# Kernel tuning notes

Measured on AMD Instinct MI355X. Metric: run time of the kernel, lower is better.

The kernel has to match this reference:

```python
import jax, jax.numpy as jnp
import numpy as np

NUM_LAYERS = 2
NUM_RES_LAYERS = 1  # residual add applied to layers i >= NUM_LAYERS - NUM_RES_LAYERS


def _lstm_seq(x, W, U, b, reverse):
    """Keras-style LSTM over full sequence. x:[B,T,E], W:[E,4H], U:[H,4H], b:[4H].
    Gate order i,f,g,o (Keras). reverse=True emulates go_backwards + K.reverse
    (lax.scan reverse=True keeps outputs time-aligned). Returns [B,T,H]."""
    B = x.shape[0]
    H = U.shape[0]
    # precompute input projections for all timesteps in one big matmul
    zx = jnp.einsum('bte,eg->btg', x, W) + b  # [B,T,4H]
    zx = jnp.swapaxes(zx, 0, 1)  # [T,B,4H]

    def step(carry, zxt):
        h, c = carry
        z = zxt + h @ U  # [B,4H]
        i, f, g, o = jnp.split(z, 4, axis=-1)
        i = jax.nn.sigmoid(i)
        f = jax.nn.sigmoid(f)
        g = jnp.tanh(g)
        o = jax.nn.sigmoid(o)
        c = f * c + i * g
        h = o * jnp.tanh(c)
        return (h, c), h

    init = (jnp.zeros((B, H), x.dtype), jnp.zeros((B, H), x.dtype))
    _, hs = jax.lax.scan(step, init, zx, reverse=reverse)  # [T,B,H]
    return jnp.swapaxes(hs, 0, 1)


def setup_inputs() -> dict:
    key = jax.random.key(0)
    k1, k2, k3 = jax.random.split(key, 3)
    B, T, E, H = 512, 200, 128, 128
    s = 0.05  # keep gates in a sane regime
    x = jax.random.normal(k1, (B, T, E), dtype=jnp.float32)
    W = jax.random.normal(k2, (NUM_LAYERS, 2, E, 4 * H), dtype=jnp.float32) * s
    U = jax.random.normal(k3, (NUM_LAYERS, 2, H, 4 * H), dtype=jnp.float32) * s
    b = jnp.ones((NUM_LAYERS, 2, 4 * H), dtype=jnp.float32)  # bias_initializer='ones'
    return {"x": x, "W": W, "U": U, "b": b}


def reference(x, W, U, b):
    # inference mode: dropout inactive
    input_fw = x
    input_bw = x
    for i in range(NUM_LAYERS):
        out_fw = _lstm_seq(input_fw, W[i, 0], U[i, 0], b[i, 0], reverse=False)
        out_bw = _lstm_seq(input_bw, W[i, 1], U[i, 1], b[i, 1], reverse=True)
        if i >= NUM_LAYERS - NUM_RES_LAYERS:
            out_fw = out_fw + input_fw
            out_bw = out_bw + input_bw
        input_fw = out_fw
        input_bw = out_bw
    # mode == 'ave'
    return (input_fw + input_bw) / 2
```

## Files before the change

kernel.cpp:

```cpp
#include <hip/hip_runtime.h>


typedef _Float16 f16;
typedef _Float16 f16x4 __attribute__((ext_vector_type(4)));
typedef _Float16 f16x8 __attribute__((ext_vector_type(8)));
typedef float    f32x4 __attribute__((ext_vector_type(4)));

#define B_   512
#define T_   200
#define E_   128
#define H_   128
#define G4_  512
#define M_   (B_*T_)

static __device__ __forceinline__ float rcpf_(float x) {
#if __has_builtin(__builtin_amdgcn_rcpf)
  return __builtin_amdgcn_rcpf(x);
#else
  return 1.f / x;
#endif
}
static __device__ __forceinline__ float sigm(float x) { return rcpf_(1.f + __expf(-x)); }
static __device__ __forceinline__ float tanh_(float x) { return 2.f * rcpf_(1.f + __expf(-2.f * x)) - 1.f; }

static __device__ __forceinline__ void lgkm_barrier() {
  asm volatile("s_waitcnt lgkmcnt(0)" ::: "memory");
  __builtin_amdgcn_s_barrier();
}

__global__ __launch_bounds__(256)
void cvt_x(const float* __restrict__ x, f16* __restrict__ xh) {
  const int n8 = M_ * E_ / 8;
  for (int i = blockIdx.x * 256 + threadIdx.x; i < n8; i += gridDim.x * 256) {
    const float4 a = ((const float4*)x)[i * 2];
    const float4 b = ((const float4*)x)[i * 2 + 1];
    f16x8 v;
    v[0] = (f16)a.x; v[1] = (f16)a.y; v[2] = (f16)a.z; v[3] = (f16)a.w;
    v[4] = (f16)b.x; v[5] = (f16)b.y; v[6] = (f16)b.z; v[7] = (f16)b.w;
    *(f16x8*)(xh + (size_t)i * 8) = v;
  }
}

__global__ __launch_bounds__(256)
void prep_w(const float* __restrict__ W, const float* __restrict__ U,
            f16* __restrict__ Wt, f16* __restrict__ Ut) {
  const int m = blockIdx.x;
  const float* s = (m < 4 ? W + (size_t)m * E_ * G4_ : U + (size_t)(m - 4) * E_ * G4_);
  f16* d        = (m < 4 ? Wt + (size_t)m * E_ * G4_ : Ut + (size_t)(m - 4) * E_ * G4_);
  for (int i = threadIdx.x; i < E_ * G4_; i += 256) {
    const int k = i >> 9, g = i & 511;
    d[(size_t)g * E_ + k] = (f16)s[i];
  }
}

template <int LAYER>
__global__ __launch_bounds__(512, 2)
void scan_fused(const f16* __restrict__ in,
                const f16* __restrict__ Utl,
                const f16* __restrict__ Wtl,
                const float* __restrict__ bl,
                const f16* __restrict__ res,
                f16* __restrict__ hout)
{
  __shared__ f16 hsh[2][16][136];

  const int tid  = threadIdx.x;
  const int lane = tid & 63;
  const int wv   = tid >> 6;
  const int row  = lane & 15;
  const int kg   = lane >> 4;
  const int bx   = blockIdx.x;
  const int dir  = bx >> 5;
  const int R0   = (bx & 31) * 16;
  const int coff = wv * 16 + kg * 4;

  const f16* Ud = Utl + (size_t)dir * G4_ * E_;
  const f16* Wd = Wtl + (size_t)dir * G4_ * E_;
  const float* bd = bl + (size_t)dir * G4_;
  const f16* ind  = in + (LAYER == 1 ? (size_t)dir * M_ * H_ : 0);
  f16* houtd      = hout + (size_t)dir * M_ * H_;

  f16x8 aU[4][4], aW[4][4];
#pragma unroll
  for (int g = 0; g < 4; ++g) {
    const size_t gcol = (size_t)(g * 128 + wv * 16 + row) * E_;
#pragma unroll
    for (int kk = 0; kk < 4; ++kk) {
      aU[g][kk] = *(const f16x8*)(Ud + gcol + kk * 32 + kg * 8);
      aW[g][kk] = *(const f16x8*)(Wd + gcol + kk * 32 + kg * 8);
    }
  }
  f32x4 zb[4];
#pragma unroll
  for (int g = 0; g < 4; ++g) {
#pragma unroll
    for (int i = 0; i < 4; ++i) zb[g][i] = bd[g * 128 + coff + i];
  }

  for (int i = tid; i < 2 * 16 * 136; i += 512) ((f16*)hsh)[i] = (f16)0.f;

  const int t0 = dir ? (T_ - 1) : 0;
  const int ts = dir ? -1 : 1;

  const f16* inrow  = ind + (size_t)(R0 + row) * T_ * E_;
  const f16* resrow = (LAYER == 1)
      ? res + (size_t)dir * M_ * H_ + (size_t)(R0 + row) * T_ * H_ : nullptr;
  f16* outrow = houtd + (size_t)(R0 + row) * T_ * H_;

  float cc[4] = {0.f, 0.f, 0.f, 0.f};

  f16x8 xA[4], xB[4];
  f16x4 rvA = {}, rvB = {};
  {
    const f16* pA = inrow + (size_t)t0 * E_;
    const f16* pB = inrow + (size_t)(t0 + ts) * E_;
#pragma unroll
    for (int kk = 0; kk < 4; ++kk) {
      xA[kk] = *(const f16x8*)(pA + kk * 32 + kg * 8);
      xB[kk] = *(const f16x8*)(pB + kk * 32 + kg * 8);
    }
    if (LAYER == 1) {
      rvA = *(const f16x4*)(resrow + (size_t)t0 * H_ + coff);
      rvB = *(const f16x4*)(resrow + (size_t)(t0 + ts) * H_ + coff);
    }
  }

  lgkm_barrier();

  auto step = [&](f16x8 (&xp)[4], f16x4& rv, int s, int rp, int wp) {
    const int t = t0 + s * ts;

    f16x8 hf[4];
#pragma unroll
    for (int kk = 0; kk < 4; ++kk) hf[kk] = *(const f16x8*)&hsh[rp][row][kk * 32 + kg * 8];

    f16x8 xf[4];
#pragma unroll
    for (int kk = 0; kk < 4; ++kk) xf[kk] = xp[kk];
    float rvf[4];
    if (LAYER == 1) {
#pragma unroll
      for (int i = 0; i < 4; ++i) rvf[i] = (float)rv[i];
    }

    {
      const int spf = s + 2;
      const size_t tpf = (spf < T_) ? (size_t)(t0 + spf * ts) : (size_t)t0;
      const f16* p = inrow + tpf * E_;
#pragma unroll
      for (int kk = 0; kk < 4; ++kk) xp[kk] = *(const f16x8*)(p + kk * 32 + kg * 8);
      if (LAYER == 1) rv = *(const f16x4*)(resrow + tpf * H_ + coff);
    }

    f32x4 z0 = zb[0], z1 = zb[1], z2 = zb[2], z3 = zb[3];
#pragma unroll
    for (int kk = 0; kk < 4; ++kk) {
      z0 = __builtin_amdgcn_mfma_f32_16x16x32_f16(aW[0][kk], xf[kk], z0, 0, 0, 0);
      z1 = __builtin_amdgcn_mfma_f32_16x16x32_f16(aW[1][kk], xf[kk], z1, 0, 0, 0);
      z2 = __builtin_amdgcn_mfma_f32_16x16x32_f16(aW[2][kk], xf[kk], z2, 0, 0, 0);
      z3 = __builtin_amdgcn_mfma_f32_16x16x32_f16(aW[3][kk], xf[kk], z3, 0, 0, 0);
    }
#pragma unroll
    for (int kk = 0; kk < 4; ++kk) {
      z0 = __builtin_amdgcn_mfma_f32_16x16x32_f16(aU[0][kk], hf[kk], z0, 0, 0, 0);
      z1 = __builtin_amdgcn_mfma_f32_16x16x32_f16(aU[1][kk], hf[kk], z1, 0, 0, 0);
      z2 = __builtin_amdgcn_mfma_f32_16x16x32_f16(aU[2][kk], hf[kk], z2, 0, 0, 0);
      z3 = __builtin_amdgcn_mfma_f32_16x16x32_f16(aU[3][kk], hf[kk], z3, 0, 0, 0);
    }

    float hv[4];
#pragma unroll
    for (int i = 0; i < 4; ++i) {
      const float ig = sigm(z0[i]);
      const float fg = sigm(z1[i]);
      const float gg = tanh_(z2[i]);
      const float og = sigm(z3[i]);
      cc[i] = fg * cc[i] + ig * gg;
      hv[i] = og * tanh_(cc[i]);
    }
    f16x4 hp;
#pragma unroll
    for (int i = 0; i < 4; ++i) hp[i] = (f16)hv[i];
    *(f16x4*)&hsh[wp][row][coff] = hp;

    f16* orow = outrow + (size_t)t * H_ + coff;
    if (LAYER == 0) {
      *(f16x4*)orow = hp;
    } else {
      f16x4 o;
#pragma unroll
      for (int i = 0; i < 4; ++i) o[i] = (f16)(0.5f * (hv[i] + rvf[i]));
      *(f16x4*)orow = o;
    }

    lgkm_barrier();
  };

  for (int k = 0; k < T_ / 2; ++k) {
    step(xA, rvA, 2 * k,     0, 1);
    step(xB, rvB, 2 * k + 1, 1, 0);
  }
}

__global__ __launch_bounds__(256)
void final_add(const f16* __restrict__ a, const f16* __restrict__ b,
               float* __restrict__ o)
{
  const int n8 = M_ * H_ / 8;
  for (int i = blockIdx.x * 256 + threadIdx.x; i < n8; i += gridDim.x * 256) {
    const f16x8 va = *(const f16x8*)(a + (size_t)i * 8);
    const f16x8 vb = *(const f16x8*)(b + (size_t)i * 8);
    float4 o0, o1;
    o0.x = (float)va[0] + (float)vb[0];  o0.y = (float)va[1] + (float)vb[1];
    o0.z = (float)va[2] + (float)vb[2];  o0.w = (float)va[3] + (float)vb[3];
    o1.x = (float)va[4] + (float)vb[4];  o1.y = (float)va[5] + (float)vb[5];
    o1.z = (float)va[6] + (float)vb[6];  o1.w = (float)va[7] + (float)vb[7];
    *(float4*)(o + (size_t)i * 8)     = o0;
    *(float4*)(o + (size_t)i * 8 + 4) = o1;
  }
}

extern "C" void kernel_launch(void* const* d_in, const int* in_sizes, int n_in,
                              void* d_out, int out_size, void* d_ws, size_t ws_size,
                              hipStream_t stream) {
  const float* x = (const float*)d_in[0];
  const float* W = (const float*)d_in[1];
  const float* U = (const float*)d_in[2];
  const float* b = (const float*)d_in[3];
  float* out = (float*)d_out;

  char* ws = (char*)d_ws;
  f16* xh = (f16*)ws;
  f16* h0 = xh + (size_t)M_ * E_;
  f16* h1 = h0 + (size_t)2 * M_ * H_;
  f16* Wt = h1 + (size_t)2 * M_ * H_;
  f16* Ut = Wt + (size_t)4 * G4_ * E_;

  const size_t WTL = (size_t)2 * G4_ * E_;
  const size_t BL  = 2 * G4_;

  cvt_x<<<dim3(2048), 256, 0, stream>>>(x, xh);
  prep_w<<<dim3(8), 256, 0, stream>>>(W, U, Wt, Ut);
  scan_fused<0><<<dim3(64), 512, 0, stream>>>(xh, Ut, Wt, b, nullptr, h0);
  scan_fused<1><<<dim3(64), 512, 0, stream>>>(h0, Ut + WTL, Wt + WTL, b + BL, h0, h1);
  final_add<<<dim3(2048), 256, 0, stream>>>(h1, h1 + (size_t)M_ * H_, out);
}
```

Before: 684.8 us.

## Replace gate transcendentals with shared-memory sigmoid LUT and pipeline input projection

Gate activations now come from an 8192-entry sigmoid lookup table in LDS, built per block, instead of exp and reciprocal. tanh is expressed as 2*sigmoid(2x)-1, with the g-gate weights and bias pre-scaled by 2. The input-projection MFMAs for the next step are issued right after the current step's recurrent MFMAs, so they sit off the serial dependency chain. The nearest-entry lookup with a 1/256 step adds approximation error and possible LDS bank conflicts, and the prefetch can read past the sequence edge, which the workspace offset seems meant to absorb.

```diff
diff --git a/kernel.cpp b/kernel.cpp
--- a/kernel.cpp
+++ b/kernel.cpp
@@ -1,4 +1,5 @@
 #include <hip/hip_runtime.h>
+#include <math.h>
 
 
 typedef _Float16 f16;
@@ -12,16 +13,7 @@
 #define H_   128
 #define G4_  512
 #define M_   (B_*T_)
-
-static __device__ __forceinline__ float rcpf_(float x) {
-#if __has_builtin(__builtin_amdgcn_rcpf)
-  return __builtin_amdgcn_rcpf(x);
-#else
-  return 1.f / x;
-#endif
-}
-static __device__ __forceinline__ float sigm(float x) { return rcpf_(1.f + __expf(-x)); }
-static __device__ __forceinline__ float tanh_(float x) { return 2.f * rcpf_(1.f + __expf(-2.f * x)) - 1.f; }
+#define LUTN 8192
 
 static __device__ __forceinline__ void lgkm_barrier() {
   asm volatile("s_waitcnt lgkmcnt(0)" ::: "memory");
@@ -49,7 +41,9 @@
   f16* d        = (m < 4 ? Wt + (size_t)m * E_ * G4_ : Ut + (size_t)(m - 4) * E_ * G4_);
   for (int i = threadIdx.x; i < E_ * G4_; i += 256) {
     const int k = i >> 9, g = i & 511;
-    d[(size_t)g * E_ + k] = (f16)s[i];
+    float v = s[i];
+    if ((g >> 7) == 2) v *= 2.f;
+    d[(size_t)g * E_ + k] = (f16)v;
   }
 }
 
@@ -62,6 +56,7 @@
                 const f16* __restrict__ res,
                 f16* __restrict__ hout)
 {
+  __shared__ float lut[LUTN];
   __shared__ f16 hsh[2][16][136];
 
   const int tid  = threadIdx.x;
@@ -80,6 +75,12 @@
   const f16* ind  = in + (LAYER == 1 ? (size_t)dir * M_ * H_ : 0);
   f16* houtd      = hout + (size_t)dir * M_ * H_;
 
+  for (int i = tid; i < LUTN; i += 512) {
+    const float xx = (float)(i - LUTN / 2) * (1.f / 256.f);
+    lut[i] = 1.f / (1.f + expf(-xx));
+  }
+  for (int i = tid; i < 2 * 16 * 136; i += 512) ((f16*)hsh)[i] = (f16)0.f;
+
   f16x8 aU[4][4], aW[4][4];
 #pragma unroll
   for (int g = 0; g < 4; ++g) {
@@ -94,10 +95,11 @@
 #pragma unroll
   for (int g = 0; g < 4; ++g) {
 #pragma unroll
-    for (int i = 0; i < 4; ++i) zb[g][i] = bd[g * 128 + coff + i];
-  }
-
-  for (int i = tid; i < 2 * 16 * 136; i += 512) ((f16*)hsh)[i] = (f16)0.f;
+    for (int i = 0; i < 4; ++i) {
+      const float v = bd[g * 128 + coff + i];
+      zb[g][i] = (g == 2) ? 2.f * v : v;
+    }
+  }
 
   const int t0 = dir ? (T_ - 1) : 0;
   const int ts = dir ? -1 : 1;
@@ -109,81 +111,92 @@
 
   float cc[4] = {0.f, 0.f, 0.f, 0.f};
 
-  f16x8 xA[4], xB[4];
+  f16x8 xP[4], xA[4], xB[4];
   f16x4 rvA = {}, rvB = {};
-  {
-    const f16* pA = inrow + (size_t)t0 * E_;
-    const f16* pB = inrow + (size_t)(t0 + ts) * E_;
+#pragma unroll
+  for (int kk = 0; kk < 4; ++kk) {
+    xP[kk] = *(const f16x8*)(inrow + (long)t0 * E_ + kk * 32 + kg * 8);
+    xA[kk] = *(const f16x8*)(inrow + (long)(t0 + ts) * E_ + kk * 32 + kg * 8);
+    xB[kk] = *(const f16x8*)(inrow + (long)(t0 + 2 * ts) * E_ + kk * 32 + kg * 8);
+  }
+  if (LAYER == 1) {
+    rvA = *(const f16x4*)(resrow + (long)t0 * H_ + coff);
+    rvB = *(const f16x4*)(resrow + (long)(t0 + ts) * H_ + coff);
+  }
+
+  lgkm_barrier();
+
+  f32x4 zA[4], zB[4];
+#pragma unroll
+  for (int g = 0; g < 4; ++g) zA[g] = zb[g];
+#pragma unroll
+  for (int kk = 0; kk < 4; ++kk) {
+    zA[0] = __builtin_amdgcn_mfma_f32_16x16x32_f16(aW[0][kk], xP[kk], zA[0], 0, 0, 0);
+    zA[1] = __builtin_amdgcn_mfma_f32_16x16x32_f16(aW[1][kk], xP[kk], zA[1], 0, 0, 0);
+    zA[2] = __builtin_amdgcn_mfma_f32_16x16x32_f16(aW[2][kk], xP[kk], zA[2], 0, 0, 0);
+    zA[3] = __builtin_amdgcn_mfma_f32_16x16x32_f16(aW[3][kk], xP[kk], zA[3], 0, 0, 0);
+  }
+
+  auto step = [&](f32x4 (&zc)[4], f32x4 (&zn)[4], f16x8 (&xn)[4], f16x4& rv,
+                  int s, int rp, int wp) {
+    const int t = t0 + s * ts;
+
+    f16x8 hf[4];
+#pragma unroll
+    for (int kk = 0; kk < 4; ++kk) hf[kk] = *(const f16x8*)&hsh[rp][row][kk * 32 + kg * 8];
+
 #pragma unroll
     for (int kk = 0; kk < 4; ++kk) {
-      xA[kk] = *(const f16x8*)(pA + kk * 32 + kg * 8);
-      xB[kk] = *(const f16x8*)(pB + kk * 32 + kg * 8);
-    }
-    if (LAYER == 1) {
-      rvA = *(const f16x4*)(resrow + (size_t)t0 * H_ + coff);
-      rvB = *(const f16x4*)(resrow + (size_t)(t0 + ts) * H_ + coff);
-    }
-  }
-
-  lgkm_barrier();
-
-  auto step = [&](f16x8 (&xp)[4], f16x4& rv, int s, int rp, int wp) {
-    const int t = t0 + s * ts;
-
-    f16x8 hf[4];
-#pragma unroll
-    for (int kk = 0; kk < 4; ++kk) hf[kk] = *(const f16x8*)&hsh[rp][row][kk * 32 + kg * 8];
-
-    f16x8 xf[4];
-#pragma unroll
-    for (int kk = 0; kk < 4; ++kk) xf[kk] = xp[kk];
+      zc[0] = __builtin_amdgcn_mfma_f32_16x16x32_f16(aU[0][kk], hf[kk], zc[0], 0, 0, 0);
+      zc[1] = __builtin_amdgcn_mfma_f32_16x16x32_f16(aU[1][kk], hf[kk], zc[1], 0, 0, 0);
+      zc[2] = __builtin_amdgcn_mfma_f32_16x16x32_f16(aU[2][kk], hf[kk], zc[2], 0, 0, 0);
+      zc[3] = __builtin_amdgcn_mfma_f32_16x16x32_f16(aU[3][kk], hf[kk], zc[3], 0, 0, 0);
+    }
+
+#pragma unroll
+    for (int g = 0; g < 4; ++g) zn[g] = zb[g];
+#pragma unroll
+    for (int kk = 0; kk < 4; ++kk) {
+      zn[0] = __builtin_amdgcn_mfma_f32_16x16x32_f16(aW[0][kk], xn[kk], zn[0], 0, 0, 0);
+      zn[1] = __builtin_amdgcn_mfma_f32_16x16x32_f16(aW[1][kk], xn[kk], zn[1], 0, 0, 0);
+      zn[2] = __builtin_amdgcn_mfma_f32_16x16x32_f16(aW[2][kk], xn[kk], zn[2], 0, 0, 0);
+      zn[3] = __builtin_amdgcn_mfma_f32_16x16x32_f16(aW[3][kk], xn[kk], zn[3], 0, 0, 0);
+    }
+
+    {
+      const f16* p = inrow + (long)(t + 3 * ts) * E_;
+#pragma unroll
+      for (int kk = 0; kk < 4; ++kk) xn[kk] = *(const f16x8*)(p + kk * 32 + kg * 8);
+    }
     float rvf[4];
     if (LAYER == 1) {
 #pragma unroll
       for (int i = 0; i < 4; ++i) rvf[i] = (float)rv[i];
-    }
-
-    {
-      const int spf = s + 2;
-      const size_t tpf = (spf < T_) ? (size_t)(t0 + spf * ts) : (size_t)t0;
-      const f16* p = inrow + tpf * E_;
-#pragma unroll
-      for (int kk = 0; kk < 4; ++kk) xp[kk] = *(const f16x8*)(p + kk * 32 + kg * 8);
-      if (LAYER == 1) rv = *(const f16x4*)(resrow + tpf * H_ + coff);
-    }
-
-    f32x4 z0 = zb[0], z1 = zb[1], z2 = zb[2], z3 = zb[3];
-#pragma unroll
-    for (int kk = 0; kk < 4; ++kk) {
-      z0 = __builtin_amdgcn_mfma_f32_16x16x32_f16(aW[0][kk], xf[kk], z0, 0, 0, 0);
-      z1 = __builtin_amdgcn_mfma_f32_16x16x32_f16(aW[1][kk], xf[kk], z1, 0, 0, 0);
-      z2 = __builtin_amdgcn_mfma_f32_16x16x32_f16(aW[2][kk], xf[kk], z2, 0, 0, 0);
-      z3 = __builtin_amdgcn_mfma_f32_16x16x32_f16(aW[3][kk], xf[kk], z3, 0, 0, 0);
-    }
-#pragma unroll
-    for (int kk = 0; kk < 4; ++kk) {
-      z0 = __builtin_amdgcn_mfma_f32_16x16x32_f16(aU[0][kk], hf[kk], z0, 0, 0, 0);
-      z1 = __builtin_amdgcn_mfma_f32_16x16x32_f16(aU[1][kk], hf[kk], z1, 0, 0, 0);
-      z2 = __builtin_amdgcn_mfma_f32_16x16x32_f16(aU[2][kk], hf[kk], z2, 0, 0, 0);
-      z3 = __builtin_amdgcn_mfma_f32_16x16x32_f16(aU[3][kk], hf[kk], z3, 0, 0, 0);
-    }
-
+      rv = *(const f16x4*)(resrow + (long)(t + 2 * ts) * H_ + coff);
+    }
+
+    auto lidx = [](float u) -> int {
+      u = fminf(fmaxf(u, 0.f), (float)(LUTN - 1));
+      return (int)u;
+    };
     float hv[4];
 #pragma unroll
     for (int i = 0; i < 4; ++i) {
-      const float ig = sigm(z0[i]);
-      const float fg = sigm(z1[i]);
-      const float gg = tanh_(z2[i]);
-      const float og = sigm(z3[i]);
+      const float ig = lut[lidx(fmaf(zc[0][i], 256.f, (float)(LUTN / 2)))];
+      const float fg = lut[lidx(fmaf(zc[1][i], 256.f, (float)(LUTN / 2)))];
+      const float gg = fmaf(2.f, lut[lidx(fmaf(zc[2][i], 256.f, (float)(LUTN / 2)))], -1.f);
+      const float og = lut[lidx(fmaf(zc[3][i], 256.f, (float)(LUTN / 2)))];
       cc[i] = fg * cc[i] + ig * gg;
-      hv[i] = og * tanh_(cc[i]);
-    }
+      const float th = fmaf(2.f, lut[lidx(fmaf(cc[i], 512.f, (float)(LUTN / 2)))], -1.f);
+      hv[i] = og * th;
+    }
+
     f16x4 hp;
 #pragma unroll
     for (int i = 0; i < 4; ++i) hp[i] = (f16)hv[i];
     *(f16x4*)&hsh[wp][row][coff] = hp;
 
-    f16* orow = outrow + (size_t)t * H_ + coff;
+    f16* orow = outrow + (long)t * H_ + coff;
     if (LAYER == 0) {
       *(f16x4*)orow = hp;
     } else {
@@ -197,8 +210,8 @@
   };
 
   for (int k = 0; k < T_ / 2; ++k) {
-    step(xA, rvA, 2 * k,     0, 1);
-    step(xB, rvB, 2 * k + 1, 1, 0);
+    step(zA, zB, xA, rvA, 2 * k,     0, 1);
+    step(zB, zA, xB, rvB, 2 * k + 1, 1, 0);
   }
 }
 
@@ -230,7 +243,7 @@
   float* out = (float*)d_out;
 
   char* ws = (char*)d_ws;
-  f16* xh = (f16*)ws;
+  f16* xh = (f16*)(ws + 2048);
   f16* h0 = xh + (size_t)M_ * E_;
   f16* h1 = h0 + (size_t)2 * M_ * H_;
   f16* Wt = h1 + (size_t)2 * M_ * H_;
```

Result: faster. 618.5 us (-9.7%).
